# Kernel optimization log

Hardware: AMD Instinct MI355X
Metric: run time of the kernel (lower is better)

The kernel has to match this reference:

```python
import jax, jax.numpy as jnp
import numpy as np
from jax import lax

B, H, W, C = 2, 256, 256, 180
WS, SH, NH = 8, 4, 6
HD = C // NH          # 30
N = WS * WS           # 64
NW = (H // WS) * (W // WS)
HID = 4 * C
SCALE = HD ** -0.5
EPS = 1e-5


def _rel_pos_index(ws):
    coords = np.stack(np.meshgrid(np.arange(ws), np.arange(ws), indexing='ij'))  # [2,ws,ws]
    cf = coords.reshape(2, -1)
    rel = (cf[:, :, None] - cf[:, None, :]).transpose(1, 2, 0)  # [N,N,2]
    rel[:, :, 0] += ws - 1
    rel[:, :, 1] += ws - 1
    rel[:, :, 0] *= 2 * ws - 1
    return rel.sum(-1)  # [N,N]


def _attn_mask(h, w, ws, sh):
    img = np.zeros((h, w))
    sl = (slice(0, -ws), slice(-ws, -sh), slice(-sh, None))
    cnt = 0
    for hs in sl:
        for wsl in sl:
            img[hs, wsl] = cnt
            cnt += 1
    mw = img.reshape(h // ws, ws, w // ws, ws).transpose(0, 2, 1, 3).reshape(-1, ws * ws)  # [nW,N]
    d = mw[:, None, :] - mw[:, :, None]  # [nW,N,N]
    return np.where(d != 0, -100.0, 0.0).astype(np.float32)


REL_IDX = jnp.asarray(_rel_pos_index(WS))          # [N,N] int
MASK = jnp.asarray(_attn_mask(H, W, WS, SH))       # [nW,N,N] float


def _ln(x, g, b):
    m = jnp.mean(x, -1, keepdims=True)
    v = jnp.mean((x - m) ** 2, -1, keepdims=True)
    return (x - m) * lax.rsqrt(v + EPS) * g + b


def _win_part(x):  # (B,H,W,C) -> (B*nW,N,C)
    x = x.reshape(B, H // WS, WS, W // WS, WS, C).transpose(0, 1, 3, 2, 4, 5)
    return x.reshape(-1, N, C)


def _win_rev(w):  # (B*nW,N,C) -> (B,H,W,C)
    x = w.reshape(B, H // WS, W // WS, WS, WS, C).transpose(0, 1, 3, 2, 4, 5)
    return x.reshape(B, H, W, C)


def setup_inputs() -> dict:
    key = jax.random.key(0)
    ks = jax.random.split(key, 8)
    s = 0.02
    return {
        'x': jax.random.normal(ks[0], (B, H * W, C), jnp.float32),
        'norm1_g': jnp.ones((C,), jnp.float32),
        'norm1_b': jnp.zeros((C,), jnp.float32),
        'qkv_w': jax.random.normal(ks[1], (C, 3 * C), jnp.float32) * s,
        'qkv_b': jnp.zeros((3 * C,), jnp.float32),
        'rel_pos_table': jax.random.normal(ks[2], ((2 * WS - 1) ** 2, NH), jnp.float32) * s,
        'proj_w': jax.random.normal(ks[3], (C, C), jnp.float32) * s,
        'proj_b': jnp.zeros((C,), jnp.float32),
        'norm2_g': jnp.ones((C,), jnp.float32),
        'norm2_b': jnp.zeros((C,), jnp.float32),
        'fc1_w': jax.random.normal(ks[4], (C, HID), jnp.float32) * s,
        'fc1_b': jnp.zeros((HID,), jnp.float32),
        'dw_w': jax.random.normal(ks[5], (HID, 1, 3, 3), jnp.float32) * s,
        'dw_b': jnp.zeros((HID,), jnp.float32),
        'fc2_w': jax.random.normal(ks[6], (HID, C), jnp.float32) * s,
        'fc2_b': jnp.zeros((C,), jnp.float32),
    }


def reference(x, norm1_g, norm1_b, qkv_w, qkv_b, rel_pos_table, proj_w, proj_b,
              norm2_g, norm2_b, fc1_w, fc1_b, dw_w, dw_b, fc2_w, fc2_b):
    shortcut = x
    h = _ln(x, norm1_g, norm1_b).reshape(B, H, W, C)
    h = jnp.roll(h, (-SH, -SH), axis=(1, 2))           # cyclic shift
    xw = _win_part(h)                                   # [B*nW, N, C]

    qkv = (xw @ qkv_w + qkv_b).reshape(-1, N, 3, NH, HD).transpose(2, 0, 3, 1, 4)
    q, k, v = qkv[0] * SCALE, qkv[1], qkv[2]            # [B_,NH,N,HD]
    attn = jnp.einsum('bhnd,bhmd->bhnm', q, k)          # [B_,NH,N,N]

    bias = rel_pos_table[REL_IDX.reshape(-1)].reshape(N, N, NH).transpose(2, 0, 1)
    attn = attn + bias[None]
    attn = attn.reshape(B, NW, NH, N, N) + MASK[None, :, None]
    attn = jax.nn.softmax(attn.reshape(-1, NH, N, N), axis=-1)

    out = jnp.einsum('bhnm,bhmd->bhnd', attn, v).transpose(0, 2, 1, 3).reshape(-1, N, C)
    out = out @ proj_w + proj_b
    out = jnp.roll(_win_rev(out), (SH, SH), axis=(1, 2)).reshape(B, H * W, C)
    x = shortcut + out

    # MLP with depthwise-conv interleave
    m = _ln(x, norm2_g, norm2_b)
    m = jax.nn.gelu(m @ fc1_w + fc1_b, approximate=False)   # [B,L,HID]
    mc = m.transpose(0, 2, 1).reshape(B, HID, H, W)
    mc = lax.conv_general_dilated(mc, dw_w, (1, 1), 'SAME',
                                  feature_group_count=HID,
                                  dimension_numbers=('NCHW', 'OIHW', 'NCHW'))
    mc = mc + dw_b[None, :, None, None]
    m = jax.nn.gelu(mc.reshape(B, HID, H * W).transpose(0, 2, 1), approximate=False)
    m = m @ fc2_w + fc2_b
    return x + m
```

## Files before the change

kernel.cpp:

```cpp
#include <hip/hip_runtime.h>
#include <hip/hip_bf16.h>


using short8 = __attribute__((ext_vector_type(8))) short;
using f32x4  = __attribute__((ext_vector_type(4))) float;

constexpr int   ROWS   = 131072;
constexpr float SCALE_ = 0.18257418583505536f;

constexpr size_t OFF_WQ    = 0;
constexpr size_t OFF_WP    = OFF_WQ   + 576*192*2;
constexpr size_t OFF_WF1   = OFF_WP   + 192*192*2;
constexpr size_t OFF_WF2T  = OFF_WF1  + 768*192*2;
constexpr size_t OFF_BQ    = OFF_WF2T + 192*768*2;
constexpr size_t OFF_BP    = OFF_BQ   + 576*4;
constexpr size_t OFF_BF1   = OFF_BP   + 192*4;
constexpr size_t OFF_BF2   = OFF_BF1  + 768*4;
constexpr size_t OFF_BIASF = OFF_BF2  + 192*4;
constexpr size_t OFF_WDWT  = OFF_BIASF + 6*4096*4;
constexpr size_t OFF_BDW   = OFF_WDWT + 9*768*4;
constexpr size_t OFF_R1    = 1048576;
constexpr size_t SZ_R      = (size_t)ROWS * 192 * 2;
constexpr size_t OFF_R2    = OFF_R1 + SZ_R;
constexpr size_t OFF_R3    = OFF_R2 + SZ_R;
constexpr size_t WS_NEEDED = OFF_R3 + SZ_R;
static_assert(OFF_BDW + 768*4 <= OFF_R1, "weights overlap R1");
static_assert((size_t)66*256*768*2 <= SZ_R, "m1 band overflows R2");

__device__ __forceinline__ unsigned short f2bf(float f) {
    __hip_bfloat16 h = __float2bfloat16(f);
    return *reinterpret_cast<unsigned short*>(&h);
}
__device__ __forceinline__ float bf2f(unsigned short u) {
    union { unsigned int i; float f; } x; x.i = ((unsigned int)u) << 16; return x.f;
}
__device__ __forceinline__ float gelu_f(float x) {
    return 0.5f * x * (1.0f + erff(x * 0.70710678118654752f));
}

__global__ __launch_bounds__(256) void prep_kernel(
    const float* __restrict__ qkv_w, const float* __restrict__ qkv_b,
    const float* __restrict__ proj_w, const float* __restrict__ proj_b,
    const float* __restrict__ fc1_w, const float* __restrict__ fc1_b,
    const float* __restrict__ fc2_w, const float* __restrict__ fc2_b,
    const float* __restrict__ rpt,
    const float* __restrict__ dw_w, const float* __restrict__ dw_b,
    unsigned short* __restrict__ wq2, unsigned short* __restrict__ wp,
    unsigned short* __restrict__ wf1, unsigned short* __restrict__ wf2t,
    float* __restrict__ bq2, float* __restrict__ bp,
    float* __restrict__ bf1, float* __restrict__ bf2,
    float* __restrict__ biasf,
    float* __restrict__ wdwT, float* __restrict__ bdw)
{
    int idx = blockIdx.x * 256 + threadIdx.x;
    constexpr int E1 = 576*192;
    constexpr int E2 = E1 + 192*192;
    constexpr int E3 = E2 + 768*192;
    constexpr int E4 = E3 + 192*768;
    constexpr int E5 = E4 + 576;
    constexpr int E6 = E5 + 192;
    constexpr int E7 = E6 + 768;
    constexpr int E8 = E7 + 192;
    constexpr int E9 = E8 + 6*4096;
    constexpr int E10 = E9 + 9*768;
    constexpr int E11 = E10 + 768;
    if (idx < E1) {
        int n = idx / 192, kx = idx % 192;
        int hh = n / 96, rem = n % 96;
        int w  = rem / 32, c = rem % 32;
        float v = 0.f;
        if (c < 30 && kx < 180) {
            v = qkv_w[kx*540 + w*180 + hh*30 + c];
            if (w == 0) v *= SCALE_;
        }
        wq2[idx] = f2bf(v);
    } else if (idx < E2) {
        int j = idx - E1; int n = j / 192, kx = j % 192;
        wp[j] = f2bf((n < 180 && kx < 180) ? proj_w[kx*180 + n] : 0.f);
    } else if (idx < E3) {
        int j = idx - E2; int n = j / 192, kx = j % 192;
        wf1[j] = f2bf((n < 720 && kx < 180) ? fc1_w[kx*720 + n] : 0.f);
    } else if (idx < E4) {
        int j = idx - E3; int n = j / 768, kx = j % 768;
        wf2t[j] = f2bf((n < 180 && kx < 720) ? fc2_w[kx*180 + n] : 0.f);
    } else if (idx < E5) {
        int n = idx - E4;
        int hh = n / 96, rem = n % 96;
        int w  = rem / 32, c = rem % 32;
        float v = 0.f;
        if (c < 30) { v = qkv_b[w*180 + hh*30 + c]; if (w == 0) v *= SCALE_; }
        bq2[n] = v;
    } else if (idx < E6) {
        int n = idx - E5; bp[n] = (n < 180) ? proj_b[n] : 0.f;
    } else if (idx < E7) {
        int n = idx - E6; bf1[n] = (n < 720) ? fc1_b[n] : 0.f;
    } else if (idx < E8) {
        int n = idx - E7; bf2[n] = (n < 180) ? fc2_b[n] : 0.f;
    } else if (idx < E9) {
        int j = idx - E8;
        int hh = j / 4096, t = j & 4095;
        int n = t >> 6, m = t & 63;
        int rid = ((n>>3) - (m>>3) + 7)*15 + ((n&7) - (m&7) + 7);
        biasf[j] = rpt[rid*6 + hh];
    } else if (idx < E10) {
        int j = idx - E9;
        int tap = j / 768, c = j % 768;
        wdwT[j] = (c < 720) ? dw_w[c*9 + tap] : 0.f;
    } else if (idx < E11) {
        int c = idx - E10;
        bdw[c] = (c < 720) ? dw_b[c] : 0.f;
    }
}

template<int ROLL>
__global__ __launch_bounds__(256) void ln_kernel(const float* __restrict__ x,
    const float* __restrict__ g, const float* __restrict__ bsh,
    unsigned short* __restrict__ out)
{
    int row  = blockIdx.x * 4 + (threadIdx.x >> 6);
    int lane = threadIdx.x & 63;
    size_t src;
    if (ROLL) {
        int b    = row >> 16;
        int widx = (row >> 6) & 1023;
        int n    = row & 63;
        int hr   = ((widx >> 5) << 3) + (n >> 3);
        int wr   = ((widx & 31) << 3) + (n & 7);
        int h2   = (hr + 4) & 255;
        int w2   = (wr + 4) & 255;
        src = ((size_t)b << 16) + (h2 << 8) + w2;
    } else {
        src = (size_t)row;
    }
    const float* xr = x + src * 180;
    float v1 = xr[lane];
    float v2 = xr[lane + 64];
    float v3 = (lane < 52) ? xr[lane + 128] : 0.0f;
    float s1 = v1 + v2 + v3;
    float s2 = v1*v1 + v2*v2 + v3*v3;
    #pragma unroll
    for (int o = 32; o > 0; o >>= 1) { s1 += __shfl_xor(s1, o); s2 += __shfl_xor(s2, o); }
    float mean = s1 * (1.0f/180.0f);
    float var  = s2 * (1.0f/180.0f) - mean*mean;
    float rstd = rsqrtf(var + 1e-5f);
    unsigned short* orow = out + (size_t)row * 192;
    orow[lane]      = f2bf((v1 - mean)*rstd*g[lane]      + bsh[lane]);
    orow[lane + 64] = f2bf((v2 - mean)*rstd*g[lane + 64] + bsh[lane + 64]);
    if (lane < 52) orow[lane + 128] = f2bf((v3 - mean)*rstd*g[lane + 128] + bsh[lane + 128]);
    else           orow[lane + 128] = 0;
}

__global__ __launch_bounds__(384, 3) void fused_qkv_attn(
    unsigned short* __restrict__ xw,
    const unsigned short* __restrict__ wq2, const float* __restrict__ bq2,
    const float* __restrict__ biasf)
{
    __shared__ __align__(16) unsigned short lds[39936];
    unsigned short* AsQ = lds;
    unsigned short* KS  = lds + 15360;
    unsigned short* VT  = lds + 27648;
    unsigned short* P   = lds;

    const int bm   = blockIdx.x;
    const int tid  = threadIdx.x;
    const int hh   = tid >> 6;
    const int lane = tid & 63;
    const int l15  = lane & 15, l4 = lane >> 4;

    {
        const unsigned short* Arow = xw + (size_t)bm * 12288;
        #pragma unroll
        for (int j = 0; j < 4; j++) {
            int c   = tid + j*384;
            int row = c / 24;
            int s   = (c % 24) * 8;
            int kt  = s >> 5, kk = s & 31;
            *(uint4*)&AsQ[kt*2560 + row*40 + kk] = *(const uint4*)&Arow[row*192 + s];
        }
    }
    __syncthreads();

    f32x4 qa[2][4];
    #pragma unroll
    for (int ct = 0; ct < 2; ct++)
        #pragma unroll
        for (int m = 0; m < 4; m++) qa[ct][m] = f32x4{0.f,0.f,0.f,0.f};
    {
        #pragma unroll
        for (int kt = 0; kt < 6; kt++) {
            short8 af[4];
            #pragma unroll
            for (int m = 0; m < 4; m++) af[m] = *(const short8*)&AsQ[kt*2560 + (m*16 + l15)*40 + l4*8];
            #pragma unroll
            for (int ct = 0; ct < 2; ct++) {
                short8 bf = *(const short8*)&wq2[(size_t)(hh*96 + ct*16 + l15)*192 + kt*32 + l4*8];
                #pragma unroll
                for (int m = 0; m < 4; m++)
                    qa[ct][m] = __builtin_amdgcn_mfma_f32_16x16x32_bf16(af[m], bf, qa[ct][m], 0, 0, 0);
            }
        }
    }
    {
        f32x4 ka[2][4];
        #pragma unroll
        for (int ct = 0; ct < 2; ct++)
            #pragma unroll
            for (int m = 0; m < 4; m++) ka[ct][m] = f32x4{0.f,0.f,0.f,0.f};
        #pragma unroll
        for (int kt = 0; kt < 6; kt++) {
            short8 af[4];
            #pragma unroll
            for (int m = 0; m < 4; m++) af[m] = *(const short8*)&AsQ[kt*2560 + (m*16 + l15)*40 + l4*8];
            #pragma unroll
            for (int ct = 0; ct < 2; ct++) {
                short8 bf = *(const short8*)&wq2[(size_t)(hh*96 + 32 + ct*16 + l15)*192 + kt*32 + l4*8];
                #pragma unroll
                for (int m = 0; m < 4; m++)
                    ka[ct][m] = __builtin_amdgcn_mfma_f32_16x16x32_bf16(af[m], bf, ka[ct][m], 0, 0, 0);
            }
        }
        #pragma unroll
        for (int ct = 0; ct < 2; ct++)
          #pragma unroll
          for (int m = 0; m < 4; m++)
            #pragma unroll
            for (int rr = 0; rr < 4; rr++) {
                int tok = m*16 + l4*4 + rr;
                int dd  = ct*16 + l15;
                KS[hh*2048 + tok*32 + dd] = f2bf(ka[ct][m][rr] + bq2[hh*96 + 32 + dd]);
            }
    }
    {
        f32x4 va[2][4];
        #pragma unroll
        for (int ct = 0; ct < 2; ct++)
            #pragma unroll
            for (int m = 0; m < 4; m++) va[ct][m] = f32x4{0.f,0.f,0.f,0.f};
        #pragma unroll
        for (int kt = 0; kt < 6; kt++) {
            short8 af[4];
            #pragma unroll
            for (int m = 0; m < 4; m++) af[m] = *(const short8*)&AsQ[kt*2560 + (m*16 + l15)*40 + l4*8];
            #pragma unroll
            for (int ct = 0; ct < 2; ct++) {
                short8 bf = *(const short8*)&wq2[(size_t)(hh*96 + 64 + ct*16 + l15)*192 + kt*32 + l4*8];
                #pragma unroll
                for (int m = 0; m < 4; m++)
                    va[ct][m] = __builtin_amdgcn_mfma_f32_16x16x32_bf16(af[m], bf, va[ct][m], 0, 0, 0);
            }
        }
        #pragma unroll
        for (int ct = 0; ct < 2; ct++)
          #pragma unroll
          for (int m = 0; m < 4; m++)
            #pragma unroll
            for (int rr = 0; rr < 4; rr++) {
                int tok = m*16 + l4*4 + rr;
                int dd  = ct*16 + l15;
                int tsw = tok ^ ((dd & 7) << 3);
                VT[hh*2048 + dd*64 + tsw] = f2bf(va[ct][m][rr] + bq2[hh*96 + 64 + dd]);
            }
    }
    __syncthreads();

    #pragma unroll
    for (int ct = 0; ct < 2; ct++)
      #pragma unroll
      for (int m = 0; m < 4; m++)
        #pragma unroll
        for (int rr = 0; rr < 4; rr++) {
            int tok = m*16 + l4*4 + rr;
            int dd  = ct*16 + l15;
            AsQ[hh*2048 + tok*32 + dd] = f2bf(qa[ct][m][rr] + bq2[hh*96 + dd]);
        }

    short8 qf[4], kf[4];
    #pragma unroll
    for (int t = 0; t < 4; t++) {
        qf[t] = *(const short8*)&AsQ[hh*2048 + (t*16 + l15)*32 + l4*8];
        kf[t] = *(const short8*)&KS [hh*2048 + (t*16 + l15)*32 + l4*8];
    }
    __syncthreads();

    f32x4 s[4][4];
    #pragma unroll
    for (int m = 0; m < 4; m++)
        #pragma unroll
        for (int n = 0; n < 4; n++)
            s[m][n] = __builtin_amdgcn_mfma_f32_16x16x32_bf16(qf[m], kf[n], f32x4{0.f,0.f,0.f,0.f}, 0, 0, 0);

    const int wi = bm & 1023;
    const int wh = wi >> 5, ww = wi & 31;
    const bool edge = (wh == 31) || (ww == 31);
    const float* bh = biasf + hh*4096;
    #pragma unroll
    for (int m = 0; m < 4; m++) {
      #pragma unroll
      for (int rr = 0; rr < 4; rr++) {
        int ni = m*16 + l4*4 + rr;
        int ln_n = 0;
        if (edge) {
            int rh = (wh < 31) ? 0 : (((ni >> 3) < 4) ? 1 : 2);
            int rw = (ww < 31) ? 0 : (((ni & 7) < 4) ? 1 : 2);
            ln_n = rh*3 + rw;
        }
        #pragma unroll
        for (int n = 0; n < 4; n++) {
            int mj = n*16 + l15;
            float add = bh[ni*64 + mj];
            if (edge) {
                int rh = (wh < 31) ? 0 : (((mj >> 3) < 4) ? 1 : 2);
                int rw = (ww < 31) ? 0 : (((mj & 7) < 4) ? 1 : 2);
                if (rh*3 + rw != ln_n) add -= 100.0f;
            }
            s[m][n][rr] += add;
        }
      }
    }
    #pragma unroll
    for (int m = 0; m < 4; m++) {
      #pragma unroll
      for (int rr = 0; rr < 4; rr++) {
        float mx = fmaxf(fmaxf(s[m][0][rr], s[m][1][rr]), fmaxf(s[m][2][rr], s[m][3][rr]));
        #pragma unroll
        for (int o = 8; o > 0; o >>= 1) mx = fmaxf(mx, __shfl_xor(mx, o));
        float sum = 0.f;
        #pragma unroll
        for (int n = 0; n < 4; n++) { float e = __expf(s[m][n][rr] - mx); s[m][n][rr] = e; sum += e; }
        #pragma unroll
        for (int o = 8; o > 0; o >>= 1) sum += __shfl_xor(sum, o);
        float inv = 1.0f / sum;
        int ni = m*16 + l4*4 + rr;
        #pragma unroll
        for (int n = 0; n < 4; n++) P[hh*4608 + ni*72 + n*16 + l15] = f2bf(s[m][n][rr] * inv);
      }
    }
    f32x4 po[4][2];
    #pragma unroll
    for (int m = 0; m < 4; m++)
        #pragma unroll
        for (int n = 0; n < 2; n++) po[m][n] = f32x4{0.f,0.f,0.f,0.f};
    #pragma unroll
    for (int ksx = 0; ksx < 2; ksx++) {
        short8 pf[4], vf[2];
        #pragma unroll
        for (int m = 0; m < 4; m++) pf[m] = *(const short8*)&P[hh*4608 + (m*16 + l15)*72 + ksx*32 + l4*8];
        #pragma unroll
        for (int n = 0; n < 2; n++) {
            int dd  = n*16 + l15;
            int g   = (ksx*4 + l4) ^ (dd & 7);
            vf[n] = *(const short8*)&VT[hh*2048 + dd*64 + g*8];
        }
        #pragma unroll
        for (int m = 0; m < 4; m++)
            #pragma unroll
            for (int n = 0; n < 2; n++)
                po[m][n] = __builtin_amdgcn_mfma_f32_16x16x32_bf16(pf[m], vf[n], po[m][n], 0, 0, 0);
    }
    unsigned short* ob = xw + (size_t)bm * 12288;
    #pragma unroll
    for (int m = 0; m < 4; m++)
      #pragma unroll
      for (int n = 0; n < 2; n++)
        #pragma unroll
        for (int rr = 0; rr < 4; rr++) {
            int ni = m*16 + l4*4 + rr;
            int dd = n*16 + l15;
            if (dd < 30) ob[ni*192 + hh*30 + dd] = f2bf(po[m][n][rr]);
        }
}

__global__ __launch_bounds__(256) void fc1_gemm64(
    const unsigned short* __restrict__ A, const unsigned short* __restrict__ Bt,
    const float* __restrict__ bias, unsigned short* __restrict__ obf)
{
    __shared__ __align__(16) unsigned short As[64*40];
    __shared__ __align__(16) unsigned short Bs[64*40];
    const int tid  = threadIdx.x;
    const int bm   = blockIdx.x, bn = blockIdx.y;
    const int lane = tid & 63;
    const int wv   = tid >> 6;
    const int wr   = wv >> 1, wc = wv & 1;
    const int l15  = lane & 15, l4 = lane >> 4;
    const int r    = tid >> 2;
    const int kk   = (tid & 3) << 3;

    f32x4 acc[2][2];
    #pragma unroll
    for (int i = 0; i < 2; i++)
        #pragma unroll
        for (int j = 0; j < 2; j++) acc[i][j] = f32x4{0.f, 0.f, 0.f, 0.f};

    const size_t abase = (size_t)(bm*64 + r) * 192 + kk;
    const size_t bbase = (size_t)(bn*64 + r) * 192 + kk;
    const int lds_wi = r*40 + kk;

    for (int kt = 0; kt < 192; kt += 32) {
        *(uint4*)&As[lds_wi] = *(const uint4*)&A[abase + kt];
        *(uint4*)&Bs[lds_wi] = *(const uint4*)&Bt[bbase + kt];
        __syncthreads();
        short8 af[2], bf[2];
        #pragma unroll
        for (int fm = 0; fm < 2; fm++) af[fm] = *(const short8*)&As[(wr*32 + fm*16 + l15)*40 + l4*8];
        #pragma unroll
        for (int fn = 0; fn < 2; fn++) bf[fn] = *(const short8*)&Bs[(wc*32 + fn*16 + l15)*40 + l4*8];
        #pragma unroll
        for (int fm = 0; fm < 2; fm++)
            #pragma unroll
            for (int fn = 0; fn < 2; fn++)
                acc[fm][fn] = __builtin_amdgcn_mfma_f32_16x16x32_bf16(af[fm], bf[fn], acc[fm][fn], 0, 0, 0);
        __syncthreads();
    }
    #pragma unroll
    for (int fm = 0; fm < 2; fm++)
      #pragma unroll
      for (int fn = 0; fn < 2; fn++)
        #pragma unroll
        for (int rr = 0; rr < 4; rr++) {
            int grow = bm*64 + wr*32 + fm*16 + l4*4 + rr;
            int gcol = bn*64 + wc*32 + fn*16 + l15;
            obf[(size_t)grow*768 + gcol] = f2bf(gelu_f(acc[fm][fn][rr] + bias[gcol]));
        }
}

template<int M_BLK, int MODE>
__global__ __launch_bounds__(256) void gemmN192(
    const unsigned short* __restrict__ A, const unsigned short* __restrict__ Bt,
    const float* __restrict__ bias, int K, int lda, int ldb,
    const float* __restrict__ xres, float* __restrict__ out)
{
    constexpr int MB = M_BLK / 16;
    constexpr int LDS_STAGE = (M_BLK*40 + 192*40) * 2;
    constexpr int LDS_CST   = M_BLK * 180 * 4;
    constexpr int LDSZ = LDS_STAGE > LDS_CST ? LDS_STAGE : LDS_CST;
    __shared__ __align__(16) char lds[LDSZ];
    unsigned short* As = (unsigned short*)lds;
    unsigned short* Bs = As + M_BLK*40;
    float* Cst = (float*)lds;

    const int tid  = threadIdx.x;
    const int bm   = blockIdx.x;
    const int lane = tid & 63;
    const int wv   = tid >> 6;
    const int l15  = lane & 15, l4 = lane >> 4;
    const int r    = tid >> 2;
    const int kk   = (tid & 3) << 3;

    f32x4 acc[MB][3];
    #pragma unroll
    for (int m = 0; m < MB; m++)
        #pragma unroll
        for (int nb = 0; nb < 3; nb++) acc[m][nb] = f32x4{0.f,0.f,0.f,0.f};

    const size_t abase = (size_t)(bm*M_BLK + r) * (size_t)lda + kk;
    const size_t bbase = (size_t)r * (size_t)ldb + kk;

    for (int kt = 0; kt < K; kt += 32) {
        if (M_BLK == 64 || tid < M_BLK*4)
            *(uint4*)&As[r*40 + kk] = *(const uint4*)&A[abase + kt];
        #pragma unroll
        for (int jj = 0; jj < 3; jj++)
            *(uint4*)&Bs[(r + jj*64)*40 + kk] = *(const uint4*)&Bt[bbase + (size_t)jj*64*ldb + kt];
        __syncthreads();
        short8 af[MB], bf[3];
        #pragma unroll
        for (int m = 0; m < MB; m++) af[m] = *(const short8*)&As[(m*16 + l15)*40 + l4*8];
        #pragma unroll
        for (int nb = 0; nb < 3; nb++) bf[nb] = *(const short8*)&Bs[(wv*48 + nb*16 + l15)*40 + l4*8];
        #pragma unroll
        for (int m = 0; m < MB; m++)
            #pragma unroll
            for (int nb = 0; nb < 3; nb++)
                acc[m][nb] = __builtin_amdgcn_mfma_f32_16x16x32_bf16(af[m], bf[nb], acc[m][nb], 0, 0, 0);
        __syncthreads();
    }

    #pragma unroll
    for (int m = 0; m < MB; m++)
      #pragma unroll
      for (int nb = 0; nb < 3; nb++)
        #pragma unroll
        for (int rr = 0; rr < 4; rr++) {
            int tok = m*16 + l4*4 + rr;
            int col = wv*48 + nb*16 + l15;
            if (col < 180) Cst[tok*180 + col] = acc[m][nb][rr];
        }
    __syncthreads();

    for (int idx = tid; idx < M_BLK*4; idx += 256) {
        int tok = idx >> 2, j = idx & 3;
        int c0  = j * 48;
        int cnt = (j == 3) ? 36 : 48;
        size_t orow;
        if (MODE == 0) {
            int grow = bm*M_BLK + tok;
            int wig  = grow >> 6;
            int b_   = wig >> 10, wi = wig & 1023, ti = grow & 63;
            int h2   = (((wi >> 5) << 3) + (ti >> 3) + 4) & 255;
            int w2   = (((wi & 31) << 3) + (ti & 7) + 4) & 255;
            orow = ((size_t)b_ << 16) + (h2 << 8) + w2;
        } else {
            orow = (size_t)(bm*M_BLK + tok);
        }
        float*       op = out  + orow*180 + c0;
        const float* cp = &Cst[tok*180 + c0];
        const float* bb = bias + c0;
        if (MODE == 0) {
            const float* xp = xres + orow*180 + c0;
            for (int i = 0; i < cnt; i += 4) {
                f32x4 ov = *(const f32x4*)&xp[i] + *(const f32x4*)&cp[i] + *(const f32x4*)&bb[i];
                *(f32x4*)&op[i] = ov;
            }
        } else {
            for (int i = 0; i < cnt; i += 4) {
                f32x4 ov = *(const f32x4*)&op[i];
                ov += *(const f32x4*)&cp[i] + *(const f32x4*)&bb[i];
                *(f32x4*)&op[i] = ov;
            }
        }
    }
}

__global__ __launch_bounds__(256) void dwconv_band(
    const unsigned short* __restrict__ m1, const float* __restrict__ wT,
    const float* __restrict__ bias, int h0, unsigned short* __restrict__ m2)
{
    const int hl  = blockIdx.x;
    const int t   = threadIdx.x;
    const int cg  = t & 31;
    const int pl  = t >> 5;
    const int w0  = blockIdx.y * 64 + pl * 8;
    const int c   = blockIdx.z * 256 + cg * 8;

    float acc[8][8];
    float bv[8];
    *(f32x4*)&bv[0] = *(const f32x4*)&bias[c];
    *(f32x4*)&bv[4] = *(const f32x4*)&bias[c + 4];
    #pragma unroll
    for (int p = 0; p < 8; p++)
        #pragma unroll
        for (int i = 0; i < 8; i++) acc[p][i] = bv[i];

    const short8 zv = {0,0,0,0,0,0,0,0};
    #pragma unroll
    for (int dh = -1; dh <= 1; dh++) {
        int hg = h0 + hl + dh;
        if (hg < 0 || hg > 255) continue;
        const unsigned short* rb = m1 + (size_t)(hl + 1 + dh) * 256 * 768 + c;
        float f[10][8];
        #pragma unroll
        for (int j = 0; j < 10; j++) {
            int w2 = w0 - 1 + j;
            short8 v = (w2 < 0 || w2 > 255) ? zv : *(const short8*)&rb[(size_t)w2*768];
            #pragma unroll
            for (int i = 0; i < 8; i++) f[j][i] = bf2f((unsigned short)v[i]);
        }
        #pragma unroll
        for (int dw2 = 0; dw2 < 3; dw2++) {
            const float* wrow = wT + ((dh+1)*3 + dw2)*768 + c;
            float wt[8];
            *(f32x4*)&wt[0] = *(const f32x4*)&wrow[0];
            *(f32x4*)&wt[4] = *(const f32x4*)&wrow[4];
            #pragma unroll
            for (int p = 0; p < 8; p++)
                #pragma unroll
                for (int i = 0; i < 8; i++)
                    acc[p][i] += f[p + dw2][i] * wt[i];
        }
    }
    unsigned short* ob = m2 + ((size_t)hl*256 + w0)*768 + c;
    #pragma unroll
    for (int p = 0; p < 8; p++) {
        short8 o;
        #pragma unroll
        for (int i = 0; i < 8; i++) o[i] = (short)f2bf(gelu_f(acc[p][i]));
        *(short8*)&ob[(size_t)p*768] = o;
    }
}

extern "C" void kernel_launch(void* const* d_in, const int* in_sizes, int n_in,
                              void* d_out, int out_size, void* d_ws, size_t ws_size,
                              hipStream_t stream) {
    (void)in_sizes; (void)n_in; (void)out_size;
    if (ws_size < WS_NEEDED) return;
    const float* x      = (const float*)d_in[0];
    const float* n1g    = (const float*)d_in[1];
    const float* n1b    = (const float*)d_in[2];
    const float* qkv_w  = (const float*)d_in[3];
    const float* qkv_b  = (const float*)d_in[4];
    const float* rpt    = (const float*)d_in[5];
    const float* proj_w = (const float*)d_in[6];
    const float* proj_b = (const float*)d_in[7];
    const float* n2g    = (const float*)d_in[8];
    const float* n2b    = (const float*)d_in[9];
    const float* fc1_w  = (const float*)d_in[10];
    const float* fc1_b  = (const float*)d_in[11];
    const float* dw_w   = (const float*)d_in[12];
    const float* dw_b   = (const float*)d_in[13];
    const float* fc2_w  = (const float*)d_in[14];
    const float* fc2_b  = (const float*)d_in[15];
    float* out = (float*)d_out;
    char*  ws  = (char*)d_ws;

    unsigned short* wq2  = (unsigned short*)(ws + OFF_WQ);
    unsigned short* wp   = (unsigned short*)(ws + OFF_WP);
    unsigned short* wf1  = (unsigned short*)(ws + OFF_WF1);
    unsigned short* wf2t = (unsigned short*)(ws + OFF_WF2T);
    float* bq2   = (float*)(ws + OFF_BQ);
    float* bp    = (float*)(ws + OFF_BP);
    float* bf1   = (float*)(ws + OFF_BF1);
    float* bf2   = (float*)(ws + OFF_BF2);
    float* biasf = (float*)(ws + OFF_BIASF);
    float* wdwT  = (float*)(ws + OFF_WDWT);
    float* bdw   = (float*)(ws + OFF_BDW);
    unsigned short* R1 = (unsigned short*)(ws + OFF_R1);
    unsigned short* R2 = (unsigned short*)(ws + OFF_R2);
    unsigned short* R3 = (unsigned short*)(ws + OFF_R3);

    prep_kernel<<<1861, 256, 0, stream>>>(qkv_w, qkv_b, proj_w, proj_b, fc1_w, fc1_b,
                                          fc2_w, fc2_b, rpt, dw_w, dw_b,
                                          wq2, wp, wf1, wf2t,
                                          bq2, bp, bf1, bf2, biasf, wdwT, bdw);
    ln_kernel<1><<<32768, 256, 0, stream>>>(x, n1g, n1b, R1);
    fused_qkv_attn<<<2048, 384, 0, stream>>>(R1, wq2, bq2, biasf);
    gemmN192<64, 0><<<2048, 256, 0, stream>>>(R1, wp, bp, 192, 192, 192, x, out);
    ln_kernel<0><<<32768, 256, 0, stream>>>(out, n2g, n2b, R1);
    for (int band = 0; band < 8; ++band) {
        const int b_img   = band >> 2;
        const int h0      = (band & 3) * 64;
        const int h_start = (h0 == 0) ? 0 : h0 - 1;
        const int h_end   = (h0 + 64 < 256) ? (h0 + 65) : 256;
        const int n_rows  = h_end - h_start;
        const int moff    = (h0 == 0) ? 1 : 0;
        const size_t arow0 = ((size_t)b_img*256 + h_start) * 256;
        const size_t pix0  = ((size_t)b_img*256 + h0) * 256;
        fc1_gemm64<<<dim3(n_rows*4, 12), 256, 0, stream>>>(
            R1 + arow0*192, wf1, bf1, R2 + (size_t)moff*256*768);
        dwconv_band<<<dim3(64, 4, 3), 256, 0, stream>>>(R2, wdwT, bdw, h0, R3);
        gemmN192<32, 1><<<512, 256, 0, stream>>>(
            R3, wf2t, bf2, 768, 768, 768, nullptr, out + pix0*180);
    }
}
```

Measured before the change: 822.2 us.

## Restructure fused window attention into two head groups to halve LDS and raise occupancy

The fused QKV+attention kernel now processes heads in two groups of three, with each pair of waves sharing a head and splitting its query rows. This cuts shared memory from about 78KB to 36KB and raises the launch-bounds occupancy target from 3 to 6 blocks. A-operands are read straight from global memory instead of being staged in LDS, XOR swizzles are added to the Q, K and P layouts, and output goes to a separate buffer (R2) whose padding columns are zeroed. The costs are more global reads of the input tile, an extra block barrier between the two groups, and recomputed mask logic per group.

After: 1.652 ms. 2.01x slower.

```diff
diff --git a/kernel.cpp b/kernel.cpp
--- a/kernel.cpp
+++ b/kernel.cpp
@@ -150,224 +150,179 @@
     else           orow[lane + 128] = 0;
 }
 
-__global__ __launch_bounds__(384, 3) void fused_qkv_attn(
-    unsigned short* __restrict__ xw,
+__global__ __launch_bounds__(384, 6) void fused_qkv_attn(
+    const unsigned short* __restrict__ xw,
+    unsigned short* __restrict__ aout,
     const unsigned short* __restrict__ wq2, const float* __restrict__ bq2,
     const float* __restrict__ biasf)
 {
-    __shared__ __align__(16) unsigned short lds[39936];
-    unsigned short* AsQ = lds;
-    unsigned short* KS  = lds + 15360;
-    unsigned short* VT  = lds + 27648;
-    unsigned short* P   = lds;
+    __shared__ __align__(16) unsigned short lds[18432];
+    unsigned short* QS = lds;
+    unsigned short* KSm = lds + 6144;
+    unsigned short* VT = lds + 12288;
+    unsigned short* P  = lds;
 
     const int bm   = blockIdx.x;
     const int tid  = threadIdx.x;
-    const int hh   = tid >> 6;
+    const int wv   = tid >> 6;
     const int lane = tid & 63;
     const int l15  = lane & 15, l4 = lane >> 4;
+    const unsigned short* Arow = xw + (size_t)bm * 12288;
+    unsigned short* ob = aout + (size_t)bm * 12288;
 
     {
-        const unsigned short* Arow = xw + (size_t)bm * 12288;
-        #pragma unroll
-        for (int j = 0; j < 4; j++) {
-            int c   = tid + j*384;
-            int row = c / 24;
-            int s   = (c % 24) * 8;
-            int kt  = s >> 5, kk = s & 31;
-            *(uint4*)&AsQ[kt*2560 + row*40 + kk] = *(const uint4*)&Arow[row*192 + s];
-        }
-    }
-    __syncthreads();
-
-    f32x4 qa[2][4];
-    #pragma unroll
-    for (int ct = 0; ct < 2; ct++)
-        #pragma unroll
-        for (int m = 0; m < 4; m++) qa[ct][m] = f32x4{0.f,0.f,0.f,0.f};
-    {
-        #pragma unroll
-        for (int kt = 0; kt < 6; kt++) {
-            short8 af[4];
-            #pragma unroll
-            for (int m = 0; m < 4; m++) af[m] = *(const short8*)&AsQ[kt*2560 + (m*16 + l15)*40 + l4*8];
-            #pragma unroll
-            for (int ct = 0; ct < 2; ct++) {
-                short8 bf = *(const short8*)&wq2[(size_t)(hh*96 + ct*16 + l15)*192 + kt*32 + l4*8];
-                #pragma unroll
-                for (int m = 0; m < 4; m++)
-                    qa[ct][m] = __builtin_amdgcn_mfma_f32_16x16x32_bf16(af[m], bf, qa[ct][m], 0, 0, 0);
-            }
-        }
-    }
-    {
-        f32x4 ka[2][4];
-        #pragma unroll
-        for (int ct = 0; ct < 2; ct++)
-            #pragma unroll
-            for (int m = 0; m < 4; m++) ka[ct][m] = f32x4{0.f,0.f,0.f,0.f};
-        #pragma unroll
-        for (int kt = 0; kt < 6; kt++) {
-            short8 af[4];
-            #pragma unroll
-            for (int m = 0; m < 4; m++) af[m] = *(const short8*)&AsQ[kt*2560 + (m*16 + l15)*40 + l4*8];
-            #pragma unroll
-            for (int ct = 0; ct < 2; ct++) {
-                short8 bf = *(const short8*)&wq2[(size_t)(hh*96 + 32 + ct*16 + l15)*192 + kt*32 + l4*8];
-                #pragma unroll
-                for (int m = 0; m < 4; m++)
-                    ka[ct][m] = __builtin_amdgcn_mfma_f32_16x16x32_bf16(af[m], bf, ka[ct][m], 0, 0, 0);
-            }
-        }
-        #pragma unroll
-        for (int ct = 0; ct < 2; ct++)
-          #pragma unroll
-          for (int m = 0; m < 4; m++)
-            #pragma unroll
-            for (int rr = 0; rr < 4; rr++) {
-                int tok = m*16 + l4*4 + rr;
-                int dd  = ct*16 + l15;
-                KS[hh*2048 + tok*32 + dd] = f2bf(ka[ct][m][rr] + bq2[hh*96 + 32 + dd]);
-            }
-    }
-    {
-        f32x4 va[2][4];
-        #pragma unroll
-        for (int ct = 0; ct < 2; ct++)
-            #pragma unroll
-            for (int m = 0; m < 4; m++) va[ct][m] = f32x4{0.f,0.f,0.f,0.f};
-        #pragma unroll
-        for (int kt = 0; kt < 6; kt++) {
-            short8 af[4];
-            #pragma unroll
-            for (int m = 0; m < 4; m++) af[m] = *(const short8*)&AsQ[kt*2560 + (m*16 + l15)*40 + l4*8];
-            #pragma unroll
-            for (int ct = 0; ct < 2; ct++) {
-                short8 bf = *(const short8*)&wq2[(size_t)(hh*96 + 64 + ct*16 + l15)*192 + kt*32 + l4*8];
-                #pragma unroll
-                for (int m = 0; m < 4; m++)
-                    va[ct][m] = __builtin_amdgcn_mfma_f32_16x16x32_bf16(af[m], bf, va[ct][m], 0, 0, 0);
-            }
-        }
-        #pragma unroll
-        for (int ct = 0; ct < 2; ct++)
-          #pragma unroll
-          for (int m = 0; m < 4; m++)
-            #pragma unroll
-            for (int rr = 0; rr < 4; rr++) {
-                int tok = m*16 + l4*4 + rr;
-                int dd  = ct*16 + l15;
-                int tsw = tok ^ ((dd & 7) << 3);
-                VT[hh*2048 + dd*64 + tsw] = f2bf(va[ct][m][rr] + bq2[hh*96 + 64 + dd]);
-            }
-    }
-    __syncthreads();
-
-    #pragma unroll
-    for (int ct = 0; ct < 2; ct++)
-      #pragma unroll
-      for (int m = 0; m < 4; m++)
-        #pragma unroll
-        for (int rr = 0; rr < 4; rr++) {
-            int tok = m*16 + l4*4 + rr;
-            int dd  = ct*16 + l15;
-            AsQ[hh*2048 + tok*32 + dd] = f2bf(qa[ct][m][rr] + bq2[hh*96 + dd]);
-        }
-
-    short8 qf[4], kf[4];
-    #pragma unroll
-    for (int t = 0; t < 4; t++) {
-        qf[t] = *(const short8*)&AsQ[hh*2048 + (t*16 + l15)*32 + l4*8];
-        kf[t] = *(const short8*)&KS [hh*2048 + (t*16 + l15)*32 + l4*8];
-    }
-    __syncthreads();
-
-    f32x4 s[4][4];
-    #pragma unroll
-    for (int m = 0; m < 4; m++)
-        #pragma unroll
-        for (int n = 0; n < 4; n++)
-            s[m][n] = __builtin_amdgcn_mfma_f32_16x16x32_bf16(qf[m], kf[n], f32x4{0.f,0.f,0.f,0.f}, 0, 0, 0);
+        int row = tid / 6, j = tid % 6;
+        *(unsigned int*)&ob[row*192 + 180 + j*2] = 0;
+    }
 
     const int wi = bm & 1023;
     const int wh = wi >> 5, ww = wi & 31;
     const bool edge = (wh == 31) || (ww == 31);
-    const float* bh = biasf + hh*4096;
-    #pragma unroll
-    for (int m = 0; m < 4; m++) {
-      #pragma unroll
-      for (int rr = 0; rr < 4; rr++) {
-        int ni = m*16 + l4*4 + rr;
-        int ln_n = 0;
-        if (edge) {
-            int rh = (wh < 31) ? 0 : (((ni >> 3) < 4) ? 1 : 2);
-            int rw = (ww < 31) ? 0 : (((ni & 7) < 4) ? 1 : 2);
-            ln_n = rh*3 + rw;
-        }
-        #pragma unroll
-        for (int n = 0; n < 4; n++) {
-            int mj = n*16 + l15;
-            float add = bh[ni*64 + mj];
+    const int h    = wv >> 1;
+    const int half = wv & 1;
+
+    for (int g = 0; g < 2; ++g) {
+        if (g) __syncthreads();
+
+        f32x4 acc[4][3];
+        #pragma unroll
+        for (int m = 0; m < 4; m++)
+            #pragma unroll
+            for (int ct = 0; ct < 3; ct++) acc[m][ct] = f32x4{0.f,0.f,0.f,0.f};
+        #pragma unroll
+        for (int kt = 0; kt < 6; kt++) {
+            short8 af[4];
+            #pragma unroll
+            for (int m = 0; m < 4; m++)
+                af[m] = *(const short8*)&Arow[(m*16 + l15)*192 + kt*32 + l4*8];
+            #pragma unroll
+            for (int ct = 0; ct < 3; ct++) {
+                int wrow = g*288 + wv*48 + ct*16 + l15;
+                short8 bf = *(const short8*)&wq2[(size_t)wrow*192 + kt*32 + l4*8];
+                #pragma unroll
+                for (int m = 0; m < 4; m++)
+                    acc[m][ct] = __builtin_amdgcn_mfma_f32_16x16x32_bf16(af[m], bf, acc[m][ct], 0, 0, 0);
+            }
+        }
+        #pragma unroll
+        for (int ct = 0; ct < 3; ct++) {
+            int gc = wv*48 + ct*16 + l15;
+            int hl = gc / 96, rem = gc % 96;
+            int which = rem >> 5, dd = rem & 31;
+            float bias = bq2[g*288 + gc];
+            #pragma unroll
+            for (int m = 0; m < 4; m++)
+                #pragma unroll
+                for (int rr = 0; rr < 4; rr++) {
+                    int tok = m*16 + l4*4 + rr;
+                    unsigned short val = f2bf(acc[m][ct][rr] + bias);
+                    if (which == 0)
+                        QS[hl*2048 + tok*32 + (dd ^ ((((tok>>1)&3))<<3))] = val;
+                    else if (which == 1)
+                        KSm[hl*2048 + tok*32 + (dd ^ ((((tok>>1)&3))<<3))] = val;
+                    else
+                        VT[hl*2048 + dd*64 + (tok ^ ((dd&7)<<3))] = val;
+                }
+        }
+        __syncthreads();
+
+        short8 qf[2], kf[4];
+        #pragma unroll
+        for (int mi = 0; mi < 2; mi++)
+            qf[mi] = *(const short8*)&QS[h*2048 + ((half*2+mi)*16 + l15)*32 + (l4 ^ ((l15>>1)&3))*8];
+        #pragma unroll
+        for (int n = 0; n < 4; n++)
+            kf[n] = *(const short8*)&KSm[h*2048 + (n*16 + l15)*32 + (l4 ^ ((l15>>1)&3))*8];
+        __syncthreads();
+
+        const int gh = g*3 + h;
+        const float* bh = biasf + gh*4096;
+        f32x4 s[2][4];
+        #pragma unroll
+        for (int mi = 0; mi < 2; mi++)
+            #pragma unroll
+            for (int n = 0; n < 4; n++)
+                s[mi][n] = __builtin_amdgcn_mfma_f32_16x16x32_bf16(qf[mi], kf[n], f32x4{0.f,0.f,0.f,0.f}, 0, 0, 0);
+        #pragma unroll
+        for (int mi = 0; mi < 2; mi++) {
+          #pragma unroll
+          for (int rr = 0; rr < 4; rr++) {
+            int ni = (half*2 + mi)*16 + l4*4 + rr;
+            int ln_n = 0;
             if (edge) {
-                int rh = (wh < 31) ? 0 : (((mj >> 3) < 4) ? 1 : 2);
-                int rw = (ww < 31) ? 0 : (((mj & 7) < 4) ? 1 : 2);
-                if (rh*3 + rw != ln_n) add -= 100.0f;
-            }
-            s[m][n][rr] += add;
-        }
-      }
-    }
-    #pragma unroll
-    for (int m = 0; m < 4; m++) {
-      #pragma unroll
-      for (int rr = 0; rr < 4; rr++) {
-        float mx = fmaxf(fmaxf(s[m][0][rr], s[m][1][rr]), fmaxf(s[m][2][rr], s[m][3][rr]));
-        #pragma unroll
-        for (int o = 8; o > 0; o >>= 1) mx = fmaxf(mx, __shfl_xor(mx, o));
-        float sum = 0.f;
-        #pragma unroll
-        for (int n = 0; n < 4; n++) { float e = __expf(s[m][n][rr] - mx); s[m][n][rr] = e; sum += e; }
-        #pragma unroll
-        for (int o = 8; o > 0; o >>= 1) sum += __shfl_xor(sum, o);
-        float inv = 1.0f / sum;
-        int ni = m*16 + l4*4 + rr;
-        #pragma unroll
-        for (int n = 0; n < 4; n++) P[hh*4608 + ni*72 + n*16 + l15] = f2bf(s[m][n][rr] * inv);
-      }
-    }
-    f32x4 po[4][2];
-    #pragma unroll
-    for (int m = 0; m < 4; m++)
-        #pragma unroll
-        for (int n = 0; n < 2; n++) po[m][n] = f32x4{0.f,0.f,0.f,0.f};
-    #pragma unroll
-    for (int ksx = 0; ksx < 2; ksx++) {
-        short8 pf[4], vf[2];
-        #pragma unroll
-        for (int m = 0; m < 4; m++) pf[m] = *(const short8*)&P[hh*4608 + (m*16 + l15)*72 + ksx*32 + l4*8];
-        #pragma unroll
-        for (int n = 0; n < 2; n++) {
-            int dd  = n*16 + l15;
-            int g   = (ksx*4 + l4) ^ (dd & 7);
-            vf[n] = *(const short8*)&VT[hh*2048 + dd*64 + g*8];
-        }
-        #pragma unroll
-        for (int m = 0; m < 4; m++)
-            #pragma unroll
-            for (int n = 0; n < 2; n++)
-                po[m][n] = __builtin_amdgcn_mfma_f32_16x16x32_bf16(pf[m], vf[n], po[m][n], 0, 0, 0);
-    }
-    unsigned short* ob = xw + (size_t)bm * 12288;
-    #pragma unroll
-    for (int m = 0; m < 4; m++)
-      #pragma unroll
-      for (int n = 0; n < 2; n++)
-        #pragma unroll
-        for (int rr = 0; rr < 4; rr++) {
-            int ni = m*16 + l4*4 + rr;
-            int dd = n*16 + l15;
-            if (dd < 30) ob[ni*192 + hh*30 + dd] = f2bf(po[m][n][rr]);
-        }
+                int rh = (wh < 31) ? 0 : (((ni >> 3) < 4) ? 1 : 2);
+                int rw = (ww < 31) ? 0 : (((ni & 7) < 4) ? 1 : 2);
+                ln_n = rh*3 + rw;
+            }
+            #pragma unroll
+            for (int n = 0; n < 4; n++) {
+                int mj = n*16 + l15;
+                float add = bh[ni*64 + mj];
+                if (edge) {
+                    int rh = (wh < 31) ? 0 : (((mj >> 3) < 4) ? 1 : 2);
+                    int rw = (ww < 31) ? 0 : (((mj & 7) < 4) ? 1 : 2);
+                    if (rh*3 + rw != ln_n) add -= 100.0f;
+                }
+                s[mi][n][rr] += add;
+            }
+          }
+        }
+        #pragma unroll
+        for (int mi = 0; mi < 2; mi++) {
+          #pragma unroll
+          for (int rr = 0; rr < 4; rr++) {
+            float mx = fmaxf(fmaxf(s[mi][0][rr], s[mi][1][rr]), fmaxf(s[mi][2][rr], s[mi][3][rr]));
+            #pragma unroll
+            for (int o = 8; o > 0; o >>= 1) mx = fmaxf(mx, __shfl_xor(mx, o));
+            float sum = 0.f;
+            #pragma unroll
+            for (int n = 0; n < 4; n++) { float e = __expf(s[mi][n][rr] - mx); s[mi][n][rr] = e; sum += e; }
+            #pragma unroll
+            for (int o = 8; o > 0; o >>= 1) sum += __shfl_xor(sum, o);
+            float inv = 1.0f / sum;
+            int ni = (half*2 + mi)*16 + l4*4 + rr;
+            #pragma unroll
+            for (int n = 0; n < 4; n++) {
+                int mj = n*16 + l15;
+                P[h*4096 + ni*64 + (mj ^ ((ni&7)<<3))] = f2bf(s[mi][n][rr] * inv);
+            }
+          }
+        }
+        f32x4 po[2][2];
+        #pragma unroll
+        for (int mi = 0; mi < 2; mi++)
+            #pragma unroll
+            for (int n2 = 0; n2 < 2; n2++) po[mi][n2] = f32x4{0.f,0.f,0.f,0.f};
+        #pragma unroll
+        for (int ksx = 0; ksx < 2; ksx++) {
+            short8 pf[2], vf[2];
+            #pragma unroll
+            for (int mi = 0; mi < 2; mi++) {
+                int row = (half*2 + mi)*16 + l15;
+                pf[mi] = *(const short8*)&P[h*4096 + row*64 + (((ksx*4 + l4) ^ (l15&7))*8)];
+            }
+            #pragma unroll
+            for (int n2 = 0; n2 < 2; n2++) {
+                int dd = n2*16 + l15;
+                vf[n2] = *(const short8*)&VT[h*2048 + dd*64 + (((ksx*4 + l4) ^ (dd&7))*8)];
+            }
+            #pragma unroll
+            for (int mi = 0; mi < 2; mi++)
+                #pragma unroll
+                for (int n2 = 0; n2 < 2; n2++)
+                    po[mi][n2] = __builtin_amdgcn_mfma_f32_16x16x32_bf16(pf[mi], vf[n2], po[mi][n2], 0, 0, 0);
+        }
+        #pragma unroll
+        for (int mi = 0; mi < 2; mi++)
+          #pragma unroll
+          for (int n2 = 0; n2 < 2; n2++)
+            #pragma unroll
+            for (int rr = 0; rr < 4; rr++) {
+                int ni = (half*2 + mi)*16 + l4*4 + rr;
+                int dd = n2*16 + l15;
+                if (dd < 30) ob[ni*192 + gh*30 + dd] = f2bf(po[mi][n2][rr]);
+            }
+    }
 }
 
 __global__ __launch_bounds__(256) void fc1_gemm64(
@@ -622,8 +577,8 @@
                                           wq2, wp, wf1, wf2t,
                                           bq2, bp, bf1, bf2, biasf, wdwT, bdw);
     ln_kernel<1><<<32768, 256, 0, stream>>>(x, n1g, n1b, R1);
-    fused_qkv_attn<<<2048, 384, 0, stream>>>(R1, wq2, bq2, biasf);
-    gemmN192<64, 0><<<2048, 256, 0, stream>>>(R1, wp, bp, 192, 192, 192, x, out);
+    fused_qkv_attn<<<2048, 384, 0, stream>>>(R1, R2, wq2, bq2, biasf);
+    gemmN192<64, 0><<<2048, 256, 0, stream>>>(R2, wp, bp, 192, 192, 192, x, out);
     ln_kernel<0><<<32768, 256, 0, stream>>>(out, n2g, n2b, R1);
     for (int band = 0; band < 8; ++band) {
         const int b_img   = band >> 2;
```

## Fuse LayerNorm2 into proj GEMM epilogue, swizzle Q/K LDS, rebalance MLP bands

Applied to the files above, without the earlier changes.

The proj GEMM epilogue now computes per-row mean and variance of the residual sum and writes the normalized bf16 row directly, which removes the separate ln_kernel pass that re-read the fp32 output. Q and K tiles in LDS get an XOR swizzle on the column index to cut bank conflicts when loading MFMA fragments. The MLP band loop changes from 8 bands of 64 rows to 10 bands of 60 rows, so m1 and m2 share one region and buffers are reassigned. The fused LayerNorm uses a single-pass E[x²]−mean² variance, which is less numerically robust than the two-pass form.

After: 912.2 us. 10.9% more time.

```diff
diff --git a/kernel.cpp b/kernel.cpp
--- a/kernel.cpp
+++ b/kernel.cpp
@@ -24,8 +24,9 @@
 constexpr size_t OFF_R2    = OFF_R1 + SZ_R;
 constexpr size_t OFF_R3    = OFF_R2 + SZ_R;
 constexpr size_t WS_NEEDED = OFF_R3 + SZ_R;
+constexpr size_t M2_SHORT_OFF = (size_t)62*256*768;
 static_assert(OFF_BDW + 768*4 <= OFF_R1, "weights overlap R1");
-static_assert((size_t)66*256*768*2 <= SZ_R, "m1 band overflows R2");
+static_assert((M2_SHORT_OFF + (size_t)60*256*768)*2 <= SZ_R, "m1+m2 overflow R3");
 
 __device__ __forceinline__ unsigned short f2bf(float f) {
     __hip_bfloat16 h = __float2bfloat16(f);
@@ -227,7 +228,7 @@
             for (int rr = 0; rr < 4; rr++) {
                 int tok = m*16 + l4*4 + rr;
                 int dd  = ct*16 + l15;
-                KS[hh*2048 + tok*32 + dd] = f2bf(ka[ct][m][rr] + bq2[hh*96 + 32 + dd]);
+                KS[hh*2048 + tok*32 + (dd ^ (((tok>>1)&3)<<3))] = f2bf(ka[ct][m][rr] + bq2[hh*96 + 32 + dd]);
             }
     }
     {
@@ -271,14 +272,14 @@
         for (int rr = 0; rr < 4; rr++) {
             int tok = m*16 + l4*4 + rr;
             int dd  = ct*16 + l15;
-            AsQ[hh*2048 + tok*32 + dd] = f2bf(qa[ct][m][rr] + bq2[hh*96 + dd]);
+            AsQ[hh*2048 + tok*32 + (dd ^ (((tok>>1)&3)<<3))] = f2bf(qa[ct][m][rr] + bq2[hh*96 + dd]);
         }
 
     short8 qf[4], kf[4];
     #pragma unroll
     for (int t = 0; t < 4; t++) {
-        qf[t] = *(const short8*)&AsQ[hh*2048 + (t*16 + l15)*32 + l4*8];
-        kf[t] = *(const short8*)&KS [hh*2048 + (t*16 + l15)*32 + l4*8];
+        qf[t] = *(const short8*)&AsQ[hh*2048 + (t*16 + l15)*32 + (l4 ^ ((l15>>1)&3))*8];
+        kf[t] = *(const short8*)&KS [hh*2048 + (t*16 + l15)*32 + (l4 ^ ((l15>>1)&3))*8];
     }
     __syncthreads();
 
@@ -427,11 +428,13 @@
 __global__ __launch_bounds__(256) void gemmN192(
     const unsigned short* __restrict__ A, const unsigned short* __restrict__ Bt,
     const float* __restrict__ bias, int K, int lda, int ldb,
-    const float* __restrict__ xres, float* __restrict__ out)
+    const float* __restrict__ xres, float* __restrict__ out,
+    const float* __restrict__ g2, const float* __restrict__ b2,
+    unsigned short* __restrict__ xn2)
 {
     constexpr int MB = M_BLK / 16;
     constexpr int LDS_STAGE = (M_BLK*40 + 192*40) * 2;
-    constexpr int LDS_CST   = M_BLK * 180 * 4;
+    constexpr int LDS_CST   = (M_BLK*180 + 16) * 4;
     constexpr int LDSZ = LDS_STAGE > LDS_CST ? LDS_STAGE : LDS_CST;
     __shared__ __align__(16) char lds[LDSZ];
     unsigned short* As = (unsigned short*)lds;
@@ -503,13 +506,34 @@
             orow = (size_t)(bm*M_BLK + tok);
         }
         float*       op = out  + orow*180 + c0;
-        const float* cp = &Cst[tok*180 + c0];
+        float*       cp = &Cst[tok*180 + c0];
         const float* bb = bias + c0;
         if (MODE == 0) {
             const float* xp = xres + orow*180 + c0;
+            float s1 = 0.f, s2 = 0.f;
             for (int i = 0; i < cnt; i += 4) {
                 f32x4 ov = *(const f32x4*)&xp[i] + *(const f32x4*)&cp[i] + *(const f32x4*)&bb[i];
                 *(f32x4*)&op[i] = ov;
+                *(f32x4*)&cp[i] = ov;
+                s1 += ov[0] + ov[1] + ov[2] + ov[3];
+                s2 += ov[0]*ov[0] + ov[1]*ov[1] + ov[2]*ov[2] + ov[3]*ov[3];
+            }
+            s1 += __shfl_xor(s1, 1); s1 += __shfl_xor(s1, 2);
+            s2 += __shfl_xor(s2, 1); s2 += __shfl_xor(s2, 2);
+            float mean = s1 * (1.0f/180.0f);
+            float rstd = rsqrtf(s2*(1.0f/180.0f) - mean*mean + 1e-5f);
+            unsigned short* xrow = xn2 + orow*192 + c0;
+            #pragma unroll
+            for (int v = 0; v < 6; v++) {
+                short8 o;
+                #pragma unroll
+                for (int e = 0; e < 8; e++) {
+                    int c = c0 + v*8 + e;
+                    float val = 0.f;
+                    if (c < 180) val = (cp[v*8 + e] - mean)*rstd*g2[c] + b2[c];
+                    o[e] = (short)f2bf(val);
+                }
+                *(short8*)&xrow[v*8] = o;
             }
         } else {
             for (int i = 0; i < cnt; i += 4) {
@@ -615,7 +639,8 @@
     float* bdw   = (float*)(ws + OFF_BDW);
     unsigned short* R1 = (unsigned short*)(ws + OFF_R1);
     unsigned short* R2 = (unsigned short*)(ws + OFF_R2);
-    unsigned short* R3 = (unsigned short*)(ws + OFF_R3);
+    unsigned short* M1 = (unsigned short*)(ws + OFF_R3);
+    unsigned short* M2 = M1 + M2_SHORT_OFF;
 
     prep_kernel<<<1861, 256, 0, stream>>>(qkv_w, qkv_b, proj_w, proj_b, fc1_w, fc1_b,
                                           fc2_w, fc2_b, rpt, dw_w, dw_b,
@@ -623,21 +648,23 @@
                                           bq2, bp, bf1, bf2, biasf, wdwT, bdw);
     ln_kernel<1><<<32768, 256, 0, stream>>>(x, n1g, n1b, R1);
     fused_qkv_attn<<<2048, 384, 0, stream>>>(R1, wq2, bq2, biasf);
-    gemmN192<64, 0><<<2048, 256, 0, stream>>>(R1, wp, bp, 192, 192, 192, x, out);
-    ln_kernel<0><<<32768, 256, 0, stream>>>(out, n2g, n2b, R1);
-    for (int band = 0; band < 8; ++band) {
-        const int b_img   = band >> 2;
-        const int h0      = (band & 3) * 64;
+    gemmN192<64, 0><<<2048, 256, 0, stream>>>(R1, wp, bp, 192, 192, 192, x, out,
+                                              n2g, n2b, R2);
+    for (int band = 0; band < 10; ++band) {
+        const int b_img   = band / 5;
+        const int h0      = (band % 5) * 60;
+        const int bh      = (h0 + 60 <= 256) ? 60 : (256 - h0);
         const int h_start = (h0 == 0) ? 0 : h0 - 1;
-        const int h_end   = (h0 + 64 < 256) ? (h0 + 65) : 256;
+        const int h_end   = (h0 + bh < 256) ? (h0 + bh + 1) : 256;
         const int n_rows  = h_end - h_start;
         const int moff    = (h0 == 0) ? 1 : 0;
         const size_t arow0 = ((size_t)b_img*256 + h_start) * 256;
         const size_t pix0  = ((size_t)b_img*256 + h0) * 256;
         fc1_gemm64<<<dim3(n_rows*4, 12), 256, 0, stream>>>(
-            R1 + arow0*192, wf1, bf1, R2 + (size_t)moff*256*768);
-        dwconv_band<<<dim3(64, 4, 3), 256, 0, stream>>>(R2, wdwT, bdw, h0, R3);
-        gemmN192<32, 1><<<512, 256, 0, stream>>>(
-            R3, wf2t, bf2, 768, 768, 768, nullptr, out + pix0*180);
-    }
-}
+            R2 + arow0*192, wf1, bf1, M1 + (size_t)moff*256*768);
+        dwconv_band<<<dim3(bh, 4, 3), 256, 0, stream>>>(M1, wdwT, bdw, h0, M2);
+        gemmN192<32, 1><<<bh*8, 256, 0, stream>>>(
+            M2, wf2t, bf2, 768, 768, 768, nullptr, out + pix0*180,
+            nullptr, nullptr, nullptr);
+    }
+}
```
